# Kernel optimization log

Measured on AMD Instinct MI355X. Metric: run time of the kernel, lower is better.

Reference implementation:

```python
import jax, jax.numpy as jnp
import numpy as np


def _next_fast_len(n):
    # smallest 5-smooth integer >= n (matches scipy.fftpack.next_fast_len)
    while True:
        m = n
        for p in (2, 3, 5):
            while m % p == 0:
                m //= p
        if m == 1:
            return n
        n += 1


def _conv1d_fft(values, weights):
    # values: [b, h, n, d], weights: [h, m]; FFT cross-correlation implementing
    # causal exponentially-decaying weighted sum (per-head EMA of values).
    N = values.shape[-2]
    M = weights.shape[-1]
    L = _next_fast_len(N + M - 1)
    f_v = jnp.fft.rfft(values, n=L, axis=-2)          # [b,h,F,d] complex
    f_w = jnp.fft.rfft(weights, n=L, axis=-1)         # [h,F]   complex
    out = jnp.fft.irfft(f_v * jnp.conj(f_w)[..., None], n=L, axis=-2)
    out = jnp.roll(out, -1, axis=-2)
    return out[..., L - N:, :]                         # [b,h,N,d]


def setup_inputs() -> dict:
    key = jax.random.key(0)
    ks = jax.random.split(key, 7)
    B, N, D, H = 4, 8192, 512, 8
    s = 1.0 / np.sqrt(D)
    return {
        "x": jax.random.normal(ks[0], (B, N, D), dtype=jnp.float32),
        "W_in": jax.random.normal(ks[1], (D, D), dtype=jnp.float32) * s,
        "b_in": jax.random.normal(ks[2], (D,), dtype=jnp.float32) * 0.01,
        "W_out": jax.random.normal(ks[3], (D, D), dtype=jnp.float32) * s,
        "b_out": jax.random.normal(ks[4], (D,), dtype=jnp.float32) * 0.01,
        "init_state": jax.random.normal(ks[5], (H, D // H), dtype=jnp.float32),
        "alpha_param": jax.random.normal(ks[6], (H,), dtype=jnp.float32),
    }


def reference(x, W_in, b_in, W_out, b_out, init_state, alpha_param):
    B, N, D = x.shape
    H, Dh = init_state.shape
    # input projection
    xp = x @ W_in.T + b_in                             # [B,N,D]
    xh = xp.reshape(B, N, H, Dh).transpose(0, 2, 1, 3)  # [B,H,N,Dh]
    # prepend learned init state, take first differences along time
    x0 = jnp.broadcast_to(init_state[None, :, None, :], (B, H, 1, Dh))
    xc = jnp.concatenate([x0, xh], axis=2)             # [B,H,N+1,Dh]
    xd = xc[:, :, 1:] - xc[:, :, :-1]                  # [B,H,N,Dh]
    # per-head smoothing coefficients
    alpha = jax.nn.sigmoid(alpha_param)[:, None]       # [H,1]
    ar = jnp.arange(N, dtype=x.dtype)
    weights = alpha * (1.0 - alpha) ** ar[::-1]        # [H,N]
    out = _conv1d_fft(xd, weights)                     # [B,H,N,Dh]
    # contribution of the initial state
    init_w = (1.0 - alpha) ** (ar + 1.0)               # [H,N]
    out = out + init_w[:, :, None] * init_state[:, None, :]
    out = out.transpose(0, 2, 1, 3).reshape(B, N, D)
    return out @ W_out.T + b_out
```

## Files before the change

kernel.cpp:

```cpp
#include <hip/hip_runtime.h>
#include <stdint.h>

#define SEQ      8192
#define BATCH    4
#define DIM      512
#define MROWS    32768
#define CHUNK    64
#define NCHUNK   128
#define NCHAN    2048
#define NHEAD    8
#define NGCHUNK  512
#define XLD      264

typedef unsigned short ushort;
typedef unsigned int   uint;
typedef __bf16 bf16x8 __attribute__((ext_vector_type(8)));
typedef float  f32x4  __attribute__((ext_vector_type(4)));
typedef ushort usx8   __attribute__((ext_vector_type(8)));

__device__ __forceinline__ ushort f2bf(float f) {
    unsigned u = __float_as_uint(f);
    unsigned r = (u + 0x7fffu + ((u >> 16) & 1u)) >> 16;
    return (ushort)r;
}
__device__ __forceinline__ float bf2f(ushort v) {
    return __uint_as_float(((unsigned)v) << 16);
}

__global__ __launch_bounds__(512, 4) void gemm1_scan_kernel(
        const float* __restrict__ x,    const float* __restrict__ W_in,
        const float* __restrict__ b_in, const float* __restrict__ W_out,
        const float* __restrict__ alpha_param,
        ushort* __restrict__ zout,      ushort* __restrict__ wout_bf,
        float* __restrict__ Lfin,       float* __restrict__ XpT)
{
    const int tid = threadIdx.x;
    const int bn  = blockIdx.x;

    if (blockIdx.y == 0) {
        const float4* src = (const float4*)W_out;
        const int n4 = (DIM * DIM) / 4;
        for (int idx = bn * 512 + tid; idx < n4; idx += 1024) {
            float4 v = src[idx];
            ushort4 r;
            r.x = f2bf(v.x); r.y = f2bf(v.y); r.z = f2bf(v.z); r.w = f2bf(v.w);
            ((ushort4*)wout_bf)[idx] = r;
        }
        return;
    }
    const int bm = blockIdx.y - 1;

    __shared__ __align__(16) char smem[2 * XLD * 128];
    ushort* As0 = (ushort*)smem;
    ushort* Bs0 = (ushort*)(smem + 16384);
    ushort* X   = (ushort*)smem;

    const int lane = tid & 63;
    const int wave = tid >> 6;
    const int wr = wave >> 2, wc = wave & 3;
    const int quad = lane >> 4, r16 = lane & 15;

    const int srow  = tid >> 2;
    const int skoff = (tid & 3) * 8;
    const float* Ag  = x    + (size_t)(bm * 128 + srow) * DIM + skoff;
    const float* Bg0 = W_in + (size_t)(bn * 256 + srow) * DIM + skoff;
    const float* Bg1 = Bg0  + (size_t)128 * DIM;

    f32x4 acc[4][4];
    #pragma unroll
    for (int i = 0; i < 4; i++)
        #pragma unroll
        for (int j = 0; j < 4; j++)
            acc[i][j] = f32x4{0.f, 0.f, 0.f, 0.f};

    const int nIter = DIM / 32;

    auto cvt8 = [&](const float* s) {
        usx8 w;
        #pragma unroll
        for (int u = 0; u < 8; u++) w[u] = f2bf(s[u]);
        return w;
    };

    {
        float a[8], b0[8], b1[8];
        #pragma unroll
        for (int u = 0; u < 8; u++) { a[u] = Ag[u]; b0[u] = Bg0[u]; b1[u] = Bg1[u]; }
        *(usx8*)&As0[tid * 8]        = cvt8(a);
        *(usx8*)&Bs0[tid * 8]        = cvt8(b0);
        *(usx8*)&Bs0[4096 + tid * 8] = cvt8(b1);
    }

    int buf = 0;
    for (int k = 0; k < nIter; ++k) {
        __syncthreads();

        float an[8], bn0[8], bn1[8];
        const bool more = (k + 1 < nIter);
        if (more) {
            const int ko = (k + 1) * 32;
            #pragma unroll
            for (int u = 0; u < 8; u++) {
                an[u]  = Ag[ko + u];
                bn0[u] = Bg0[ko + u];
                bn1[u] = Bg1[ko + u];
            }
        }

        bf16x8 af[4], bfr[4];
        #pragma unroll
        for (int i = 0; i < 4; i++)
            af[i] = *(const bf16x8*)&As0[buf * 4096 + (wr * 64 + i * 16 + r16) * 32 + quad * 8];
        #pragma unroll
        for (int j = 0; j < 4; j++)
            bfr[j] = *(const bf16x8*)&Bs0[buf * 8192 + (wc * 64 + j * 16 + r16) * 32 + quad * 8];

        #pragma unroll
        for (int i = 0; i < 4; i++)
            #pragma unroll
            for (int j = 0; j < 4; j++)
                acc[i][j] = __builtin_amdgcn_mfma_f32_16x16x32_bf16(
                                bfr[j], af[i], acc[i][j], 0, 0, 0);

        if (more) {
            const int nb = buf ^ 1;
            *(usx8*)&As0[nb * 4096 + tid * 8]        = cvt8(an);
            *(usx8*)&Bs0[nb * 8192 + tid * 8]        = cvt8(bn0);
            *(usx8*)&Bs0[nb * 8192 + 4096 + tid * 8] = cvt8(bn1);
        }
        buf ^= 1;
    }

    __syncthreads();
    #pragma unroll
    for (int i = 0; i < 4; i++) {
        const int ml = wr * 64 + i * 16 + r16;
        #pragma unroll
        for (int j = 0; j < 4; j++) {
            const int nl = wc * 64 + j * 16 + quad * 4;
            const float4 bv = *(const float4*)&b_in[bn * 256 + nl];
            ushort4 r4;
            r4.x = f2bf(acc[i][j][0] + bv.x);
            r4.y = f2bf(acc[i][j][1] + bv.y);
            r4.z = f2bf(acc[i][j][2] + bv.z);
            r4.w = f2bf(acc[i][j][3] + bv.w);
            *(ushort4*)&X[ml * XLD + nl] = r4;
        }
    }
    __syncthreads();

    const int chalf = tid >> 8;
    const int cidx  = tid & 255;
    const int g     = 2 * bm + chalf;
    const int d     = bn * 256 + cidx;
    const int h     = d >> 6;
    const float alpha = 1.0f / (1.0f + expf(-alpha_param[h]));
    const float c     = 1.0f - alpha;

    const ushort* Xr  = X + chalf * 64 * XLD + cidx;
    ushort* zrow = zout + ((size_t)(bm * 128 + chalf * 64)) * DIM + d;

    float z = 0.f, prev = 0.f;
    #pragma unroll 8
    for (int r = 0; r < CHUNK; ++r) {
        float xv = bf2f(Xr[r * XLD]);
        z = c * z + alpha * (xv - prev);
        prev = xv;
        zrow[(size_t)r * DIM] = f2bf(z);
    }
    Lfin[(size_t)g * 512 + d]       = z;
    XpT[(size_t)(g + 1) * 512 + d]  = prev;
}

__global__ void scan_fixg_kernel(const float* __restrict__ Lfin,
                                 const float* __restrict__ XpT,
                                 const float* __restrict__ alpha_param,
                                 const float* __restrict__ init_state,
                                 float* __restrict__ G)
{
    int ch = blockIdx.x * blockDim.x + threadIdx.x;
    if (ch >= NCHAN) return;
    const int b = ch >> 9;
    const int d = ch & (DIM - 1);
    const int h = d >> 6;
    const float alpha = 1.0f / (1.0f + expf(-alpha_param[h]));
    const float c = 1.0f - alpha;
    const float c2 = c * c, c4 = c2 * c2, c8 = c4 * c4,
                c16 = c8 * c8, c32 = c16 * c16;
    const float c63 = c32 * c16 * c8 * c4 * c2 * c;
    const float sinit = init_state[d];

    float Z = sinit;
    const float* Lp = Lfin + (size_t)(b * NCHUNK) * 512 + d;
    const float* Xp = XpT  + (size_t)(b * NCHUNK) * 512 + d;
    float*       Gp = G    + (size_t)(b * NCHUNK) * 512 + d;

    constexpr int PF = 16;
    float Lr[PF], Xr[PF];
    #pragma unroll
    for (int j = 0; j < PF; ++j) {
        Lr[j] = Lp[(size_t)j * 512];
        Xr[j] = Xp[(size_t)j * 512];
    }
    for (int gr = 0; gr < NCHUNK / PF; ++gr) {
        #pragma unroll
        for (int j = 0; j < PF; ++j) {
            const int kl = gr * PF + j;
            const float xpt = (kl == 0) ? sinit : Xr[j];
            const float Lc  = Lr[j];
            if (gr + 1 < NCHUNK / PF) {
                Lr[j] = Lp[(size_t)((gr + 1) * PF + j) * 512];
                Xr[j] = Xp[(size_t)((gr + 1) * PF + j) * 512];
            }
            const float Gv = c * Z - alpha * xpt;
            Gp[(size_t)kl * 512] = Gv;
            Z = Lc + c63 * Gv;
        }
    }
}

#define GLDS(g, l) __builtin_amdgcn_global_load_lds(                        \
        (const __attribute__((address_space(1))) void*)(g),                 \
        (__attribute__((address_space(3))) void*)(l), 16, 0, 0)

__global__ __launch_bounds__(512, 4) void gemm2_kernel(
        const ushort* __restrict__ Az, const ushort* __restrict__ Bw,
        const float* __restrict__ bias, float* __restrict__ Cout,
        const float* __restrict__ G, const float* __restrict__ alpha_param)
{
    __shared__ __align__(16) ushort As[2][128 * 32];
    __shared__ __align__(16) ushort Bs[2][256 * 32];

    const int tid  = threadIdx.x;
    const int lane = tid & 63;
    const int wave = tid >> 6;
    const int wr = wave >> 2, wc = wave & 3;
    const int bm = blockIdx.y, bn = blockIdx.x;
    const int quad = lane >> 4, r16 = lane & 15;

    const int srow  = tid >> 2;
    const int skoff = (tid & 3) * 8;
    const ushort* Ag16 = Az + (size_t)(bm * 128 + srow) * DIM + skoff;
    const ushort* Bg0  = Bw + (size_t)(bn * 256 + srow) * DIM + skoff;
    const ushort* Bg1  = Bg0 + (size_t)128 * DIM;

    const int m   = bm * 128 + srow;
    const int tau = m & (CHUNK - 1);
    const float* Gc = G + (size_t)(m >> 6) * 512;
    const float t1 = (float)tau;
    float fc0,fc1,fc2,fc3,fc4,fc5,fc6,fc7;
    {
        float a, c;
        a = 1.f/(1.f+expf(-alpha_param[0])); c = 1.f - a; fc0 = exp2f(t1 * log2f(c));
        a = 1.f/(1.f+expf(-alpha_param[1])); c = 1.f - a; fc1 = exp2f(t1 * log2f(c));
        a = 1.f/(1.f+expf(-alpha_param[2])); c = 1.f - a; fc2 = exp2f(t1 * log2f(c));
        a = 1.f/(1.f+expf(-alpha_param[3])); c = 1.f - a; fc3 = exp2f(t1 * log2f(c));
        a = 1.f/(1.f+expf(-alpha_param[4])); c = 1.f - a; fc4 = exp2f(t1 * log2f(c));
        a = 1.f/(1.f+expf(-alpha_param[5])); c = 1.f - a; fc5 = exp2f(t1 * log2f(c));
        a = 1.f/(1.f+expf(-alpha_param[6])); c = 1.f - a; fc6 = exp2f(t1 * log2f(c));
        a = 1.f/(1.f+expf(-alpha_param[7])); c = 1.f - a; fc7 = exp2f(t1 * log2f(c));
    }
    auto selfac = [&](int hh) -> float {
        float f = fc0;
        f = (hh == 1) ? fc1 : f;
        f = (hh == 2) ? fc2 : f;
        f = (hh == 3) ? fc3 : f;
        f = (hh == 4) ? fc4 : f;
        f = (hh == 5) ? fc5 : f;
        f = (hh == 6) ? fc6 : f;
        f = (hh == 7) ? fc7 : f;
        return f;
    };
    auto fixpack = [&](usx8 av, float4 z0, float4 z1, float fac) {
        usx8 w;
        w[0] = f2bf(bf2f(av[0]) + fac * z0.x);
        w[1] = f2bf(bf2f(av[1]) + fac * z0.y);
        w[2] = f2bf(bf2f(av[2]) + fac * z0.z);
        w[3] = f2bf(bf2f(av[3]) + fac * z0.w);
        w[4] = f2bf(bf2f(av[4]) + fac * z1.x);
        w[5] = f2bf(bf2f(av[5]) + fac * z1.y);
        w[6] = f2bf(bf2f(av[6]) + fac * z1.z);
        w[7] = f2bf(bf2f(av[7]) + fac * z1.w);
        return w;
    };

    f32x4 acc[4][4];
    #pragma unroll
    for (int i = 0; i < 4; i++)
        #pragma unroll
        for (int j = 0; j < 4; j++)
            acc[i][j] = f32x4{0.f, 0.f, 0.f, 0.f};

    const int nIter = DIM / 32;

    auto stageB = [&](int k0, int b) {
        GLDS(Bg0 + k0, &Bs[b][tid * 8]);
        GLDS(Bg1 + k0, &Bs[b][128 * 32 + tid * 8]);
    };

    stageB(0, 0);
    {
        usx8 av = *(const usx8*)(Ag16);
        float4 z0 = *(const float4*)&Gc[skoff];
        float4 z1 = *(const float4*)&Gc[skoff + 4];
        *(usx8*)&As[0][tid * 8] = fixpack(av, z0, z1, selfac(skoff >> 6));
    }

    int buf = 0;
    for (int k = 0; k < nIter; ++k) {
        __syncthreads();

        usx8 av_n; float4 zn0, zn1; float fac_n = 0.f;
        const bool more = (k + 1 < nIter);
        if (more) {
            const int ko = (k + 1) * 32;
            stageB(ko, buf ^ 1);
            av_n = *(const usx8*)(Ag16 + ko);
            const int dbase = ko + skoff;
            zn0 = *(const float4*)&Gc[dbase];
            zn1 = *(const float4*)&Gc[dbase + 4];
            fac_n = selfac(dbase >> 6);
        }

        bf16x8 af[4], bfr[4];
        #pragma unroll
        for (int i = 0; i < 4; i++)
            af[i] = *(const bf16x8*)&As[buf][(wr * 64 + i * 16 + r16) * 32 + quad * 8];
        #pragma unroll
        for (int j = 0; j < 4; j++)
            bfr[j] = *(const bf16x8*)&Bs[buf][(wc * 64 + j * 16 + r16) * 32 + quad * 8];

        #pragma unroll
        for (int i = 0; i < 4; i++)
            #pragma unroll
            for (int j = 0; j < 4; j++)
                acc[i][j] = __builtin_amdgcn_mfma_f32_16x16x32_bf16(
                                bfr[j], af[i], acc[i][j], 0, 0, 0);

        if (more)
            *(usx8*)&As[buf ^ 1][tid * 8] = fixpack(av_n, zn0, zn1, fac_n);
        buf ^= 1;
    }

    #pragma unroll
    for (int i = 0; i < 4; i++) {
        const int mr = bm * 128 + wr * 64 + i * 16 + r16;
        #pragma unroll
        for (int j = 0; j < 4; j++) {
            const int n0 = bn * 256 + wc * 64 + j * 16 + quad * 4;
            const float4 bv = *(const float4*)&bias[n0];
            float4 v = make_float4(acc[i][j][0] + bv.x, acc[i][j][1] + bv.y,
                                   acc[i][j][2] + bv.z, acc[i][j][3] + bv.w);
            *(float4*)&Cout[(size_t)mr * DIM + n0] = v;
        }
    }
}

extern "C" void kernel_launch(void* const* d_in, const int* in_sizes, int n_in,
                              void* d_out, int out_size, void* d_ws, size_t ws_size,
                              hipStream_t stream) {
    const float* x           = (const float*)d_in[0];
    const float* W_in        = (const float*)d_in[1];
    const float* b_in        = (const float*)d_in[2];
    const float* W_out       = (const float*)d_in[3];
    const float* b_out       = (const float*)d_in[4];
    const float* init_state  = (const float*)d_in[5];
    const float* alpha_param = (const float*)d_in[6];
    float* out = (float*)d_out;

    ushort* z_bf    = (ushort*)d_ws;
    ushort* wout_bf = z_bf + (size_t)MROWS * DIM;
    float*  Lfin    = (float*)(wout_bf + (size_t)DIM * DIM);
    float*  XpT     = Lfin + (size_t)NGCHUNK * 512;
    float*  G       = XpT  + (size_t)(NGCHUNK + 1) * 512;

    dim3 g1(2, MROWS / 128 + 1);
    gemm1_scan_kernel<<<g1, 512, 0, stream>>>(
        x, W_in, b_in, W_out, alpha_param, z_bf, wout_bf, Lfin, XpT);

    scan_fixg_kernel<<<NCHAN / 256, 256, 0, stream>>>(
        Lfin, XpT, alpha_param, init_state, G);

    dim3 g2(2, MROWS / 128);
    gemm2_kernel<<<g2, 512, 0, stream>>>(
        z_bf, wout_bf, b_out, out, G, alpha_param);
}
```

Before: 202.0 us.

## Pre-convert both weight matrices to bf16 and stage W_in via direct global-to-LDS loads

A separate small kernel now converts W_in and W_out to bf16 before the first GEMM, replacing the extra block row that converted only W_out. The first GEMM loads its B operand as bf16 straight into LDS with global_load_lds, so it no longer re-reads and re-converts fp32 W_in in every block, which halves that traffic and frees registers. The float-to-bf16 helper also switches to the compiler's native conversion. The cost is one more kernel launch and a small extra workspace buffer.

```diff
diff --git a/kernel.cpp b/kernel.cpp
--- a/kernel.cpp
+++ b/kernel.cpp
@@ -19,42 +19,46 @@
 typedef ushort usx8   __attribute__((ext_vector_type(8)));
 
 __device__ __forceinline__ ushort f2bf(float f) {
-    unsigned u = __float_as_uint(f);
-    unsigned r = (u + 0x7fffu + ((u >> 16) & 1u)) >> 16;
-    return (ushort)r;
+    union { __bf16 h; ushort u; } cv;
+    cv.h = (__bf16)f;
+    return cv.u;
 }
 __device__ __forceinline__ float bf2f(ushort v) {
     return __uint_as_float(((unsigned)v) << 16);
 }
 
+__global__ void weights_to_bf16_kernel(const float* __restrict__ w_in,
+                                       const float* __restrict__ w_out,
+                                       ushort* __restrict__ dst, int n4each) {
+    int i = blockIdx.x * blockDim.x + threadIdx.x;
+    if (i >= 2 * n4each) return;
+    const float4* src = (i < n4each) ? (const float4*)w_in
+                                     : (const float4*)w_out - n4each;
+    float4 v = src[i];
+    ushort4 r;
+    r.x = f2bf(v.x); r.y = f2bf(v.y); r.z = f2bf(v.z); r.w = f2bf(v.w);
+    ((ushort4*)dst)[i] = r;
+}
+
+#define GLDS(g, l) __builtin_amdgcn_global_load_lds(                        \
+        (const __attribute__((address_space(1))) void*)(g),                 \
+        (__attribute__((address_space(3))) void*)(l), 16, 0, 0)
+
 __global__ __launch_bounds__(512, 4) void gemm1_scan_kernel(
-        const float* __restrict__ x,    const float* __restrict__ W_in,
-        const float* __restrict__ b_in, const float* __restrict__ W_out,
-        const float* __restrict__ alpha_param,
-        ushort* __restrict__ zout,      ushort* __restrict__ wout_bf,
+        const float* __restrict__ x,    const ushort* __restrict__ Bw,
+        const float* __restrict__ b_in, const float* __restrict__ alpha_param,
+        ushort* __restrict__ zout,
         float* __restrict__ Lfin,       float* __restrict__ XpT)
 {
-    const int tid = threadIdx.x;
-    const int bn  = blockIdx.x;
-
-    if (blockIdx.y == 0) {
-        const float4* src = (const float4*)W_out;
-        const int n4 = (DIM * DIM) / 4;
-        for (int idx = bn * 512 + tid; idx < n4; idx += 1024) {
-            float4 v = src[idx];
-            ushort4 r;
-            r.x = f2bf(v.x); r.y = f2bf(v.y); r.z = f2bf(v.z); r.w = f2bf(v.w);
-            ((ushort4*)wout_bf)[idx] = r;
-        }
-        return;
-    }
-    const int bm = blockIdx.y - 1;
-
     __shared__ __align__(16) char smem[2 * XLD * 128];
     ushort* As0 = (ushort*)smem;
     ushort* Bs0 = (ushort*)(smem + 16384);
     ushort* X   = (ushort*)smem;
 
+    const int tid = threadIdx.x;
+    const int bn  = blockIdx.x;
+    const int bm  = blockIdx.y;
+
     const int lane = tid & 63;
     const int wave = tid >> 6;
     const int wr = wave >> 2, wc = wave & 3;
@@ -62,9 +66,9 @@
 
     const int srow  = tid >> 2;
     const int skoff = (tid & 3) * 8;
-    const float* Ag  = x    + (size_t)(bm * 128 + srow) * DIM + skoff;
-    const float* Bg0 = W_in + (size_t)(bn * 256 + srow) * DIM + skoff;
-    const float* Bg1 = Bg0  + (size_t)128 * DIM;
+    const float*  Ag  = x  + (size_t)(bm * 128 + srow) * DIM + skoff;
+    const ushort* Bg0 = Bw + (size_t)(bn * 256 + srow) * DIM + skoff;
+    const ushort* Bg1 = Bg0 + (size_t)128 * DIM;
 
     f32x4 acc[4][4];
     #pragma unroll
@@ -75,6 +79,10 @@
 
     const int nIter = DIM / 32;
 
+    auto stageB = [&](int k0, int b) {
+        GLDS(Bg0 + k0, &Bs0[b * 8192 + tid * 8]);
+        GLDS(Bg1 + k0, &Bs0[b * 8192 + 4096 + tid * 8]);
+    };
     auto cvt8 = [&](const float* s) {
         usx8 w;
         #pragma unroll
@@ -82,29 +90,25 @@
         return w;
     };
 
+    stageB(0, 0);
     {
-        float a[8], b0[8], b1[8];
-        #pragma unroll
-        for (int u = 0; u < 8; u++) { a[u] = Ag[u]; b0[u] = Bg0[u]; b1[u] = Bg1[u]; }
-        *(usx8*)&As0[tid * 8]        = cvt8(a);
-        *(usx8*)&Bs0[tid * 8]        = cvt8(b0);
-        *(usx8*)&Bs0[4096 + tid * 8] = cvt8(b1);
+        float a[8];
+        #pragma unroll
+        for (int u = 0; u < 8; u++) a[u] = Ag[u];
+        *(usx8*)&As0[tid * 8] = cvt8(a);
     }
 
     int buf = 0;
     for (int k = 0; k < nIter; ++k) {
         __syncthreads();
 
-        float an[8], bn0[8], bn1[8];
+        float an[8];
         const bool more = (k + 1 < nIter);
         if (more) {
             const int ko = (k + 1) * 32;
+            stageB(ko, buf ^ 1);
             #pragma unroll
-            for (int u = 0; u < 8; u++) {
-                an[u]  = Ag[ko + u];
-                bn0[u] = Bg0[ko + u];
-                bn1[u] = Bg1[ko + u];
-            }
+            for (int u = 0; u < 8; u++) an[u] = Ag[ko + u];
         }
 
         bf16x8 af[4], bfr[4];
@@ -122,12 +126,8 @@
                 acc[i][j] = __builtin_amdgcn_mfma_f32_16x16x32_bf16(
                                 bfr[j], af[i], acc[i][j], 0, 0, 0);
 
-        if (more) {
-            const int nb = buf ^ 1;
-            *(usx8*)&As0[nb * 4096 + tid * 8]        = cvt8(an);
-            *(usx8*)&Bs0[nb * 8192 + tid * 8]        = cvt8(bn0);
-            *(usx8*)&Bs0[nb * 8192 + 4096 + tid * 8] = cvt8(bn1);
-        }
+        if (more)
+            *(usx8*)&As0[(buf ^ 1) * 4096 + tid * 8] = cvt8(an);
         buf ^= 1;
     }
 
@@ -219,10 +219,6 @@
     }
 }
 
-#define GLDS(g, l) __builtin_amdgcn_global_load_lds(                        \
-        (const __attribute__((address_space(1))) void*)(g),                 \
-        (__attribute__((address_space(3))) void*)(l), 16, 0, 0)
-
 __global__ __launch_bounds__(512, 4) void gemm2_kernel(
         const ushort* __restrict__ Az, const ushort* __restrict__ Bw,
         const float* __restrict__ bias, float* __restrict__ Cout,
@@ -369,14 +365,19 @@
     float* out = (float*)d_out;
 
     ushort* z_bf    = (ushort*)d_ws;
-    ushort* wout_bf = z_bf + (size_t)MROWS * DIM;
+    ushort* win_bf  = z_bf   + (size_t)MROWS * DIM;
+    ushort* wout_bf = win_bf + (size_t)DIM * DIM;
     float*  Lfin    = (float*)(wout_bf + (size_t)DIM * DIM);
     float*  XpT     = Lfin + (size_t)NGCHUNK * 512;
     float*  G       = XpT  + (size_t)(NGCHUNK + 1) * 512;
 
-    dim3 g1(2, MROWS / 128 + 1);
+    const int nw4 = (DIM * DIM) / 4;
+    weights_to_bf16_kernel<<<(2 * nw4 + 255) / 256, 256, 0, stream>>>(
+        W_in, W_out, win_bf, nw4);
+
+    dim3 g1(2, MROWS / 128);
     gemm1_scan_kernel<<<g1, 512, 0, stream>>>(
-        x, W_in, b_in, W_out, alpha_param, z_bf, wout_bf, Lfin, XpT);
+        x, win_bf, b_in, alpha_param, z_bf, Lfin, XpT);
 
     scan_fixg_kernel<<<NCHAN / 256, 256, 0, stream>>>(
         Lfin, XpT, alpha_param, init_state, G);
```

Result: faster. 196.5 us (-2.7%).
